# Kernel optimization log

Measured on AMD Instinct MI355X. Metric: run time of the kernel, lower is better.

## Reference

```python
import jax, jax.numpy as jnp
import numpy as np

B, C_IN, H, W = 4, 128, 32, 128   # W must equal out_channels (fc_out acts on last dim)
C_OUT, NUM_HEADS = 128, 2
BN_EPS = 1e-5


def setup_inputs() -> dict:
    key = jax.random.key(0)
    ks = jax.random.split(key, 14)
    s = 0.05  # small init scale for weights
    d = {
        "x": jax.random.normal(ks[0], (B, C_IN, H, W), jnp.float32),
        "wq": jax.random.normal(ks[1], (C_OUT, C_IN), jnp.float32) * s,
        "bq": jax.random.normal(ks[2], (C_OUT,), jnp.float32) * s,
        "wk": jax.random.normal(ks[3], (C_OUT, C_IN), jnp.float32) * s,
        "bk": jax.random.normal(ks[4], (C_OUT,), jnp.float32) * s,
        "wv": jax.random.normal(ks[5], (C_OUT, C_IN), jnp.float32) * s,
        "bv": jax.random.normal(ks[6], (C_OUT,), jnp.float32) * s,
        "fc_w": jax.random.normal(ks[7], (C_OUT, C_OUT), jnp.float32) * s,
        "fc_b": jax.random.normal(ks[8], (C_OUT,), jnp.float32) * s,
        "bn_gamma": jnp.ones((C_OUT,), jnp.float32),
        "bn_beta": jnp.zeros((C_OUT,), jnp.float32),
        "bn_mean": jax.random.normal(ks[9], (C_OUT,), jnp.float32) * 0.1,
        "bn_var": jax.random.uniform(ks[10], (C_OUT,), jnp.float32, 0.5, 1.5),
        "prelu_a": jnp.full((1,), 0.25, jnp.float32),
    }
    return d


def reference(x, wq, bq, wk, bk, wv, bv, fc_w, fc_b,
              bn_gamma, bn_beta, bn_mean, bn_var, prelu_a):
    b, c_in, h, w = x.shape
    c_out = wq.shape[0]
    nh = NUM_HEADS
    dk = c_out // nh
    L = h * w
    xf = x.reshape(b, c_in, L)                                # (B, Cin, L)
    # 1x1 convs == per-token linear projections
    q = jnp.einsum('oi,bil->bol', wq, xf) + bq[:, None]       # (B, Cout, L)
    k = jnp.einsum('oi,bil->bol', wk, xf) + bk[:, None]
    v = jnp.einsum('oi,bil->bol', wv, xf) + bv[:, None]
    Q = q.reshape(b, nh, dk, L)                               # (B, h, d_k, L)
    K = k.reshape(b, nh, dk, L)
    V = v.reshape(b, nh, dk, L)
    # scaled dot-product attention over the L = H*W tokens
    scores = jnp.einsum('bhdl,bhdm->bhlm', Q, K) / jnp.sqrt(jnp.float32(dk))
    attn = jax.nn.softmax(scores, axis=-1)                    # (B, h, L, L)
    out = jnp.einsum('bhlm,bhdm->bhdl', attn, V)              # (B, h, d_k, L)
    out = out.reshape(b, c_out, h, w)                         # (B, Cout, H, W)
    # fc_out: torch Linear on the LAST dim (W == Cout)
    y = jnp.einsum('bchw,ow->bcho', out, fc_w) + fc_b         # (B, Cout, H, W)
    # BatchNorm2d (eval mode: running stats) over channel dim
    inv = jax.lax.rsqrt(bn_var + BN_EPS)
    y = (y - bn_mean[None, :, None, None]) * (inv * bn_gamma)[None, :, None, None] \
        + bn_beta[None, :, None, None]
    # PReLU (single shared slope); dropout is identity in eval
    y = jnp.where(y > 0, y, prelu_a[0] * y)
    return y
```

## Files before the change

### kernel.cpp

```cpp
#include <hip/hip_runtime.h>

typedef _Float16 f16x8 __attribute__((ext_vector_type(8)));
typedef _Float16 f16x4t __attribute__((ext_vector_type(4)));
typedef __fp16 h16x2 __attribute__((ext_vector_type(2)));
typedef float f32x4 __attribute__((ext_vector_type(4)));
typedef float f32x16 __attribute__((ext_vector_type(16)));
typedef unsigned int uint2v __attribute__((ext_vector_type(2)));

#define L_SZ 4096

__device__ __forceinline__ unsigned short f2h(float f) {
    _Float16 h = (_Float16)f;
    return __builtin_bit_cast(unsigned short, h);
}
__device__ __forceinline__ unsigned int pk2(float a, float b) {
    h16x2 p = __builtin_amdgcn_cvt_pkrtz(a, b);
    return __builtin_bit_cast(unsigned int, p);
}
__device__ __forceinline__ float fexp2(float x) {
#if __has_builtin(__builtin_amdgcn_exp2f)
    return __builtin_amdgcn_exp2f(x);
#else
    return exp2f(x);
#endif
}
__device__ __forceinline__ float frcp(float x) {
#if __has_builtin(__builtin_amdgcn_rcpf)
    return __builtin_amdgcn_rcpf(x);
#else
    return 1.0f / x;
#endif
}
__device__ __forceinline__ void async16(unsigned short* lds, const unsigned short* g) {
    __builtin_amdgcn_global_load_lds(
        (const __attribute__((address_space(1))) unsigned int*)g,
        (__attribute__((address_space(3))) unsigned int*)lds, 16, 0, 0);
}

#define SLOT(row, ci) ((((ci) * 64) + ((row) & 32) + (((row) & 31) ^ (ci))) * 8)

__global__ __launch_bounds__(256, 3) void qkv_kernel(
    const float* __restrict__ x,
    const float* __restrict__ wq, const float* __restrict__ wk,
    const float* __restrict__ wv,
    const float* __restrict__ bq, const float* __restrict__ bk,
    const float* __restrict__ bv,
    unsigned short* __restrict__ Qp, unsigned short* __restrict__ Kp,
    unsigned short* __restrict__ Vp)
{
    int raw = blockIdx.x;
    int v = (raw & 7) * 96 + (raw >> 3);
    int tile = v / 3;
    int p = v - tile * 3;
    int bidx = tile >> 6;
    int l0 = (tile & 63) * 64;
    int tid = threadIdx.x;
    int wave = tid >> 6, lane = tid & 63;
    int c = lane & 15, qd = lane >> 4;

    __shared__ __align__(16) unsigned short Ws[128 * 128];
    __shared__ __align__(16) unsigned short Sc[9216];

    const float* wsrc = (p == 0) ? wq : (p == 1 ? wk : wv);
    #pragma unroll
    for (int t = 0; t < 32; ++t) {
        int e2 = tid + t * 256;
        float2 wv2 = *(const float2*)&wsrc[e2 * 2];
        int e = e2 * 2;
        int o = e >> 7, ci = (e & 127) >> 3, j = e & 7;
        *(unsigned int*)&Ws[o * 128 + ((ci ^ (o & 15)) * 8) + j] = pk2(wv2.x, wv2.y);
    }

    unsigned short* Xs = Sc;
    #pragma unroll
    for (int it = 0; it < 8; ++it) {
        int i  = (tid >> 4) + 16 * it;
        int l4 = (tid & 15) * 4;
        const float4 vx = *(const float4*)&x[(bidx * 128 + i) * L_SZ + l0 + l4];
        float vv[4] = {vx.x, vx.y, vx.z, vx.w};
        int ci = i >> 3;
        #pragma unroll
        for (int u = 0; u < 4; ++u) {
            int l = l4 + u;
            Xs[l * 128 + ((ci ^ (l & 15)) * 8) + (i & 7)] = f2h(vv[u]);
        }
    }
    __syncthreads();

    f16x8 afrag[4];
    #pragma unroll
    for (int kc = 0; kc < 4; ++kc) {
        int l = wave * 16 + c;
        int ci = kc * 4 + qd;
        afrag[kc] = *(const f16x8*)&Xs[l * 128 + ((ci ^ (l & 15)) * 8)];
    }
    __syncthreads();

    f32x4 acc[8];
    #pragma unroll
    for (int nt = 0; nt < 8; ++nt) acc[nt] = (f32x4){0.f, 0.f, 0.f, 0.f};

    #pragma unroll
    for (int kc = 0; kc < 4; ++kc) {
        #pragma unroll
        for (int nt = 0; nt < 8; ++nt) {
            int o = nt * 16 + c;
            f16x8 bfrag = *(const f16x8*)&Ws[o * 128 + (((kc * 4 + qd) ^ c) * 8)];
            acc[nt] = __builtin_amdgcn_mfma_f32_16x16x32_f16(afrag[kc], bfrag, acc[nt], 0, 0, 0);
        }
    }

    const float s_q = 0.18033688011f;
    if (p == 0) {
        #pragma unroll
        for (int nt = 0; nt < 8; ++nt) {
            int o = nt * 16 + c;
            int h = o >> 6, d = o & 63;
            #pragma unroll
            for (int r = 0; r < 4; ++r) {
                int l = l0 + wave * 16 + qd * 4 + r;
                Qp[((bidx * 2 + h) * L_SZ + l) * 64 + d] = f2h((acc[nt][r] + bq[o]) * s_q);
            }
        }
    } else if (p == 1) {
        #pragma unroll
        for (int nt = 0; nt < 8; ++nt) {
            int o = nt * 16 + c;
            int h = o >> 6, d = o & 63;
            #pragma unroll
            for (int r = 0; r < 4; ++r) {
                int l = l0 + wave * 16 + qd * 4 + r;
                Kp[((bidx * 2 + h) * L_SZ + l) * 64 + d] = f2h(acc[nt][r] + bk[o]);
            }
        }
    } else {
        unsigned short* Vt = Sc;
        #pragma unroll
        for (int nt = 0; nt < 8; ++nt) {
            int o = nt * 16 + c;
            #pragma unroll
            for (int r = 0; r < 4; ++r) {
                int ll = wave * 16 + qd * 4 + r;
                Vt[o * 72 + ll] = f2h(acc[nt][r] + bv[o]);
            }
        }
        __syncthreads();
        #pragma unroll
        for (int t = 0; t < 2; ++t) {
            int u = tid + t * 256;
            int row = u >> 2;
            int lc = (u & 3) * 16;
            uint4 a0 = *(const uint4*)&Vt[row * 72 + lc];
            uint4 a1 = *(const uint4*)&Vt[row * 72 + lc + 8];
            *(uint4*)&Vp[(size_t)(bidx * 128 + row) * L_SZ + l0 + lc] = a0;
            *(uint4*)&Vp[(size_t)(bidx * 128 + row) * L_SZ + l0 + lc + 8] = a1;
        }
    }
}

__global__ __launch_bounds__(256, 4) void attn_kernel(
    const unsigned short* __restrict__ Qp, const unsigned short* __restrict__ Kp,
    const unsigned short* __restrict__ Vp,
    unsigned short* __restrict__ Opart, float* __restrict__ Mpart, float* __restrict__ Lpart)
{
    int raw = blockIdx.x;
    int blk = (raw & 7) * 128 + (raw >> 3);
    int lt = blk & 31;
    int bh = (blk >> 5) & 7;
    int sp = blk >> 8;
    int l0 = lt * 128;
    int tid = threadIdx.x;
    int wave = tid >> 6, lane = tid & 63;
    int ln = lane & 31, hi = lane >> 5;
    int b = bh >> 1, h = bh & 1;

    __shared__ __align__(16) unsigned short Ks[2][4096];
    __shared__ __align__(16) unsigned short Vs[2][4096];

    const unsigned short* Qb = Qp + (size_t)bh * L_SZ * 64;
    const unsigned short* Kb = Kp + (size_t)bh * L_SZ * 64;
    const unsigned short* Vb = Vp + ((size_t)b * 128 + h * 64) * L_SZ;

    int lq = l0 + wave * 32 + ln;
    f16x8 qf[4];
    #pragma unroll
    for (int kc = 0; kc < 4; ++kc)
        qf[kc] = *(const f16x8*)&Qb[(size_t)lq * 64 + kc * 16 + hi * 8];

    float m_st = -1e30f, lsum = 0.f;
    f32x16 acc0 = {}, acc1 = {};

    int mglob = sp * 1024;
    int ci0 = wave, ci1 = 4 + wave;
    int r0_ = (lane & 32) | ((lane & 31) ^ ci0);
    int r1_ = (lane & 32) | ((lane & 31) ^ ci1);

#define STAGE(t, buf) do {                                                        \
        int m0_ = mglob + (t) * 64;                                               \
        async16(&Ks[buf][(wave * 64) * 8],       &Kb[(size_t)(m0_ + r0_) * 64 + ci0 * 8]); \
        async16(&Ks[buf][(256 + wave * 64) * 8], &Kb[(size_t)(m0_ + r1_) * 64 + ci1 * 8]); \
        async16(&Vs[buf][(wave * 64) * 8],       &Vb[(size_t)r0_ * L_SZ + m0_ + ci0 * 8]); \
        async16(&Vs[buf][(256 + wave * 64) * 8], &Vb[(size_t)r1_ * L_SZ + m0_ + ci1 * 8]); \
    } while (0)

    STAGE(0, 0);

    for (int it = 0; it < 16; ++it) {
        int cur = it & 1;
        __syncthreads();
        if (it < 15) STAGE(it + 1, cur ^ 1);

        __builtin_amdgcn_s_setprio(1);
        f32x16 s0 = {}, s1 = {};
        #pragma unroll
        for (int kc = 0; kc < 4; ++kc) {
            int cd = kc * 2 + hi;
            f16x8 k0 = *(const f16x8*)&Ks[cur][SLOT(ln, cd)];
            f16x8 k1 = *(const f16x8*)&Ks[cur][SLOT(32 + ln, cd)];
            s0 = __builtin_amdgcn_mfma_f32_32x32x16_f16(k0, qf[kc], s0, 0, 0, 0);
            s1 = __builtin_amdgcn_mfma_f32_32x32x16_f16(k1, qf[kc], s1, 0, 0, 0);
        }

        float t[8];
        #pragma unroll
        for (int r = 0; r < 8; ++r)
            t[r] = fmaxf(fmaxf(s0[r], s0[r + 8]), s1[r]);
        #pragma unroll
        for (int r = 0; r < 4; ++r)
            t[r] = fmaxf(fmaxf(t[r], t[r + 4]), s1[8 + r]);
        float m01 = fmaxf(fmaxf(t[0], t[1]), s1[12]);
        float m23 = fmaxf(fmaxf(t[2], t[3]), s1[13]);
        float mx = fmaxf(fmaxf(m01, m23), fmaxf(s1[14], s1[15]));
        mx = fmaxf(mx, __shfl_xor(mx, 32));

        if (!__all(mx <= m_st + 8.0f)) {
            float mnew = fmaxf(m_st, mx);
            float alpha = fexp2(m_st - mnew);
            m_st = mnew;
            lsum *= alpha;
            #pragma unroll
            for (int r = 0; r < 16; ++r) { acc0[r] *= alpha; acc1[r] *= alpha; }
        }
        float rs0 = 0.f, rs1 = 0.f, rs2 = 0.f, rs3 = 0.f;
        #pragma unroll
        for (int r = 0; r < 4; ++r) {
            float p0 = fexp2(s0[r]      - m_st); s0[r]      = p0; rs0 += p0;
            float p1 = fexp2(s0[r + 4]  - m_st); s0[r + 4]  = p1; rs1 += p1;
            float p2 = fexp2(s0[r + 8]  - m_st); s0[r + 8]  = p2; rs2 += p2;
            float p3 = fexp2(s0[r + 12] - m_st); s0[r + 12] = p3; rs3 += p3;
        }
        #pragma unroll
        for (int r = 0; r < 4; ++r) {
            float p0 = fexp2(s1[r]      - m_st); s1[r]      = p0; rs0 += p0;
            float p1 = fexp2(s1[r + 4]  - m_st); s1[r + 4]  = p1; rs1 += p1;
            float p2 = fexp2(s1[r + 8]  - m_st); s1[r + 8]  = p2; rs2 += p2;
            float p3 = fexp2(s1[r + 12] - m_st); s1[r + 12] = p3; rs3 += p3;
        }
        lsum += (rs0 + rs1) + (rs2 + rs3);

        #pragma unroll
        for (int kc = 0; kc < 4; ++kc) {
            unsigned int a0, a1, a2, a3;
            if (kc == 0) {
                a0 = pk2(s0[0], s0[1]);  a1 = pk2(s0[2], s0[3]);
                a2 = pk2(s0[4], s0[5]);  a3 = pk2(s0[6], s0[7]);
            } else if (kc == 1) {
                a0 = pk2(s0[8], s0[9]);  a1 = pk2(s0[10], s0[11]);
                a2 = pk2(s0[12], s0[13]); a3 = pk2(s0[14], s0[15]);
            } else if (kc == 2) {
                a0 = pk2(s1[0], s1[1]);  a1 = pk2(s1[2], s1[3]);
                a2 = pk2(s1[4], s1[5]);  a3 = pk2(s1[6], s1[7]);
            } else {
                a0 = pk2(s1[8], s1[9]);  a1 = pk2(s1[10], s1[11]);
                a2 = pk2(s1[12], s1[13]); a3 = pk2(s1[14], s1[15]);
            }
            uint2v r02 = __builtin_amdgcn_permlane32_swap(a0, a2, false, false);
            uint2v r13 = __builtin_amdgcn_permlane32_swap(a1, a3, false, false);
            uint4 pw; pw.x = r02[0]; pw.y = r13[0]; pw.z = r02[1]; pw.w = r13[1];
            f16x8 pf = __builtin_bit_cast(f16x8, pw);
            int cd = kc * 2 + hi;
            f16x8 v0 = *(const f16x8*)&Vs[cur][SLOT(ln, cd)];
            f16x8 v1 = *(const f16x8*)&Vs[cur][SLOT(32 + ln, cd)];
            acc0 = __builtin_amdgcn_mfma_f32_32x32x16_f16(v0, pf, acc0, 0, 0, 0);
            acc1 = __builtin_amdgcn_mfma_f32_32x32x16_f16(v1, pf, acc1, 0, 0, 0);
        }
        __builtin_amdgcn_s_setprio(0);
    }
#undef STAGE

    float l_tot = lsum + __shfl_xor(lsum, 32);
    unsigned short* Ow = Opart + (size_t)(sp * 8 + bh) * 64 * 4096;
    #pragma unroll
    for (int r = 0; r < 16; ++r) {
        int d0 = (r & 3) + 8 * (r >> 2) + 4 * hi;
        Ow[(size_t)d0 * 4096 + lq] = f2h(acc0[r]);
        Ow[(size_t)(32 + d0) * 4096 + lq] = f2h(acc1[r]);
    }
    if (hi == 0) {
        Mpart[(sp * 8 + bh) * 4096 + lq] = m_st;
        Lpart[(sp * 8 + bh) * 4096 + lq] = l_tot;
    }
}

__global__ __launch_bounds__(256, 2) void fc_kernel(
    const unsigned short* __restrict__ Opart, const float* __restrict__ Mp,
    const float* __restrict__ Lp, const float* __restrict__ fcw_f,
    const float* __restrict__ fc_b, const float* __restrict__ bn_g,
    const float* __restrict__ bn_b, const float* __restrict__ bn_m,
    const float* __restrict__ bn_v, const float* __restrict__ prelu_a,
    float* __restrict__ out)
{
    int raw = blockIdx.x;
    int blk = (raw & 7) * 64 + (raw >> 3);
    int r0 = blk * 32;
    int tid = threadIdx.x;
    int c0 = blk & 127;
    int bh = blk >> 6;
    int d = c0 & 63;

    int wave = tid >> 6, lane = tid & 63;
    int c = lane & 15, qd = lane >> 4;
    int rw = r0 + (wave >> 1) * 16;
    int o0 = (wave & 1) * 64;
    int hh = (rw + c) & 31;

    __shared__ __align__(16) unsigned short Fw[128 * 128];
    __shared__ __align__(16) unsigned short SclU[4096 * 4];

    uint4 ovr[4][4];
    #pragma unroll
    for (int kc = 0; kc < 4; ++kc) {
        int w0 = kc * 32 + qd * 8;
        #pragma unroll
        for (int s = 0; s < 4; ++s)
            ovr[kc][s] = *(const uint4*)&Opart[(size_t)(s * 8 + bh) * 262144 + (size_t)d * 4096 + hh * 128 + w0];
    }

    #pragma unroll
    for (int t = 0; t < 16; ++t) {
        int l = tid + t * 256;
        float m0 = Mp[(0 * 8 + bh) * 4096 + l], m1 = Mp[(1 * 8 + bh) * 4096 + l];
        float m2 = Mp[(2 * 8 + bh) * 4096 + l], m3 = Mp[(3 * 8 + bh) * 4096 + l];
        float mx = fmaxf(fmaxf(m0, m1), fmaxf(m2, m3));
        float a0 = fexp2(m0 - mx), a1 = fexp2(m1 - mx);
        float a2 = fexp2(m2 - mx), a3 = fexp2(m3 - mx);
        float den = a0 * Lp[(0 * 8 + bh) * 4096 + l] + a1 * Lp[(1 * 8 + bh) * 4096 + l]
                  + a2 * Lp[(2 * 8 + bh) * 4096 + l] + a3 * Lp[(3 * 8 + bh) * 4096 + l];
        float inv = frcp(den);
        int hl = l >> 7, ww = l & 127;
        int slot = hl * 128 + ((ww + hl) & 127);
        uint2 sc;
        sc.x = pk2(a0 * inv, a1 * inv);
        sc.y = pk2(a2 * inv, a3 * inv);
        *(uint2*)&SclU[slot * 4] = sc;
    }
    #pragma unroll
    for (int t = 0; t < 32; ++t) {
        int e2 = tid + t * 256;
        float2 v = *(const float2*)&fcw_f[e2 * 2];
        int e = e2 * 2;
        int o = e >> 7, ci = (e & 127) >> 3, j = e & 7;
        *(unsigned int*)&Fw[o * 128 + ((ci ^ (o & 15)) * 8) + j] = pk2(v.x, v.y);
    }
    __syncthreads();

    f16x8 af[4];
    #pragma unroll
    for (int kc = 0; kc < 4; ++kc) {
        int w0 = kc * 32 + qd * 8;
        f16x8 ov0 = __builtin_bit_cast(f16x8, ovr[kc][0]);
        f16x8 ov1 = __builtin_bit_cast(f16x8, ovr[kc][1]);
        f16x8 ov2 = __builtin_bit_cast(f16x8, ovr[kc][2]);
        f16x8 ov3 = __builtin_bit_cast(f16x8, ovr[kc][3]);
        #pragma unroll
        for (int j = 0; j < 8; ++j) {
            int slot = hh * 128 + ((w0 + j + hh) & 127);
            f16x4t sc = *(const f16x4t*)&SclU[slot * 4];
            float v = (float)ov0[j] * (float)sc[0] + (float)ov1[j] * (float)sc[1]
                    + (float)ov2[j] * (float)sc[2] + (float)ov3[j] * (float)sc[3];
            af[kc][j] = (_Float16)v;
        }
    }

    f32x4 acc[4];
    #pragma unroll
    for (int nt = 0; nt < 4; ++nt) acc[nt] = (f32x4){0.f, 0.f, 0.f, 0.f};
    #pragma unroll
    for (int kc = 0; kc < 4; ++kc) {
        #pragma unroll
        for (int nt = 0; nt < 4; ++nt) {
            int o = o0 + nt * 16 + c;
            f16x8 bf = *(const f16x8*)&Fw[o * 128 + (((kc * 4 + qd) ^ c) * 8)];
            acc[nt] = __builtin_amdgcn_mfma_f32_16x16x32_f16(af[kc], bf, acc[nt], 0, 0, 0);
        }
    }

    float pa = prelu_a[0];
    float g  = bn_g[c0] * rsqrtf(bn_v[c0] + 1e-5f);
    float mn = bn_m[c0], bt = bn_b[c0];
    #pragma unroll
    for (int r = 0; r < 4; ++r) {
        int orow = rw + qd * 4 + r;
        #pragma unroll
        for (int nt = 0; nt < 4; ++nt) {
            int o = o0 + nt * 16 + c;
            float y = (acc[nt][r] + fc_b[o] - mn) * g + bt;
            y = y > 0.f ? y : pa * y;
            out[(size_t)orow * 128 + o] = y;
        }
    }
}

extern "C" void kernel_launch(void* const* d_in, const int* in_sizes, int n_in,
                              void* d_out, int out_size, void* d_ws, size_t ws_size,
                              hipStream_t stream) {
    const float* x     = (const float*)d_in[0];
    const float* wq    = (const float*)d_in[1];
    const float* bq    = (const float*)d_in[2];
    const float* wk    = (const float*)d_in[3];
    const float* bk    = (const float*)d_in[4];
    const float* wv    = (const float*)d_in[5];
    const float* bv    = (const float*)d_in[6];
    const float* fcw_f = (const float*)d_in[7];
    const float* fcb   = (const float*)d_in[8];
    const float* bn_g  = (const float*)d_in[9];
    const float* bn_b  = (const float*)d_in[10];
    const float* bn_m  = (const float*)d_in[11];
    const float* bn_v  = (const float*)d_in[12];
    const float* pa    = (const float*)d_in[13];
    float* out = (float*)d_out;

    unsigned short* Qp  = (unsigned short*)d_ws;
    unsigned short* Kp  = Qp + 8 * L_SZ * 64;
    unsigned short* Vp  = Kp + 8 * L_SZ * 64;
    unsigned short* Opart = Vp + 8 * L_SZ * 64;
    float* Mpart = (float*)(Opart + 4 * 8 * 64 * L_SZ);
    float* Lpart = Mpart + 4 * 8 * L_SZ;

    hipLaunchKernelGGL(qkv_kernel,  dim3(768),  dim3(256), 0, stream,
                       x, wq, wk, wv, bq, bk, bv, Qp, Kp, Vp);
    hipLaunchKernelGGL(attn_kernel, dim3(1024), dim3(256), 0, stream,
                       Qp, Kp, Vp, Opart, Mpart, Lpart);
    hipLaunchKernelGGL(fc_kernel,   dim3(512),  dim3(256), 0, stream,
                       Opart, Mpart, Lpart, fcw_f, fcb, bn_g, bn_b, bn_m, bn_v, pa, out);
}
```

Measured before the change: 158.5 us.

## Precompute fp16 weight and softmax-scale images in prep kernels, async-load into LDS

Adds a prep kernel that converts the QKV and fc weights to swizzled fp16 images once, and a scl_kernel that computes the per-split softmax merge scales once per (batch, head). qkv_kernel and fc_kernel now copy these images into LDS with global_load_lds async copies instead of redundantly converting fp32 data in every block. Q/K outputs are staged through LDS so they can be written with coalesced 16-byte stores. This adds two extra kernel launches and some workspace traffic.

```diff
diff --git a/kernel.cpp b/kernel.cpp
--- a/kernel.cpp
+++ b/kernel.cpp
@@ -39,10 +39,29 @@
 
 #define SLOT(row, ci) ((((ci) * 64) + ((row) & 32) + (((row) & 31) ^ (ci))) * 8)
 
+__global__ __launch_bounds__(256) void prep_kernel(
+    const float* __restrict__ wq, const float* __restrict__ wk,
+    const float* __restrict__ wv, const float* __restrict__ fcw,
+    unsigned short* __restrict__ Wimg, unsigned short* __restrict__ Fimg)
+{
+    int e2 = blockIdx.x * 256 + threadIdx.x;
+    if (e2 < 24576) {
+        const float* src = (e2 < 8192) ? wq : (e2 < 16384 ? wk : wv);
+        float2 v = *(const float2*)&src[(e2 * 2) & 16383];
+        int e = e2 * 2;
+        int o = e >> 7, ci = (e & 127) >> 3, j = e & 7;
+        *(unsigned int*)&Wimg[o * 128 + ((ci ^ (o & 15)) * 8) + j] = pk2(v.x, v.y);
+    } else {
+        int fe = (e2 - 24576) * 2;
+        float2 v = *(const float2*)&fcw[fe];
+        int o = fe >> 7, ci = (fe & 127) >> 3, j = fe & 7;
+        *(unsigned int*)&Fimg[o * 128 + ((ci ^ (o & 15)) * 8) + j] = pk2(v.x, v.y);
+    }
+}
+
 __global__ __launch_bounds__(256, 3) void qkv_kernel(
     const float* __restrict__ x,
-    const float* __restrict__ wq, const float* __restrict__ wk,
-    const float* __restrict__ wv,
+    const unsigned short* __restrict__ Wimg,
     const float* __restrict__ bq, const float* __restrict__ bk,
     const float* __restrict__ bv,
     unsigned short* __restrict__ Qp, unsigned short* __restrict__ Kp,
@@ -61,15 +80,10 @@
     __shared__ __align__(16) unsigned short Ws[128 * 128];
     __shared__ __align__(16) unsigned short Sc[9216];
 
-    const float* wsrc = (p == 0) ? wq : (p == 1 ? wk : wv);
-    #pragma unroll
-    for (int t = 0; t < 32; ++t) {
-        int e2 = tid + t * 256;
-        float2 wv2 = *(const float2*)&wsrc[e2 * 2];
-        int e = e2 * 2;
-        int o = e >> 7, ci = (e & 127) >> 3, j = e & 7;
-        *(unsigned int*)&Ws[o * 128 + ((ci ^ (o & 15)) * 8) + j] = pk2(wv2.x, wv2.y);
-    }
+    const unsigned short* wsrc = Wimg + p * 16384;
+    #pragma unroll
+    for (int t = 0; t < 8; ++t)
+        async16(&Ws[(t * 256 + wave * 64) * 8], &wsrc[(size_t)(t * 256 + wave * 64 + lane) * 8]);
 
     unsigned short* Xs = Sc;
     #pragma unroll
@@ -111,27 +125,30 @@
     }
 
     const float s_q = 0.18033688011f;
-    if (p == 0) {
+    if (p < 2) {
+        const float* bias = (p == 0) ? bq : bk;
+        unsigned short* Ot = Sc;
         #pragma unroll
         for (int nt = 0; nt < 8; ++nt) {
             int o = nt * 16 + c;
-            int h = o >> 6, d = o & 63;
+            float bo = bias[o];
             #pragma unroll
             for (int r = 0; r < 4; ++r) {
-                int l = l0 + wave * 16 + qd * 4 + r;
-                Qp[((bidx * 2 + h) * L_SZ + l) * 64 + d] = f2h((acc[nt][r] + bq[o]) * s_q);
+                int ll = wave * 16 + qd * 4 + r;
+                float val = acc[nt][r] + bo;
+                if (p == 0) val *= s_q;
+                Ot[ll * 144 + o] = f2h(val);
             }
         }
-    } else if (p == 1) {
-        #pragma unroll
-        for (int nt = 0; nt < 8; ++nt) {
-            int o = nt * 16 + c;
-            int h = o >> 6, d = o & 63;
-            #pragma unroll
-            for (int r = 0; r < 4; ++r) {
-                int l = l0 + wave * 16 + qd * 4 + r;
-                Kp[((bidx * 2 + h) * L_SZ + l) * 64 + d] = f2h(acc[nt][r] + bk[o]);
-            }
+        __syncthreads();
+        unsigned short* dst = (p == 0) ? Qp : Kp;
+        #pragma unroll
+        for (int t = 0; t < 4; ++t) {
+            int u = tid + t * 256;
+            int row = u >> 4, col = (u & 15) * 8;
+            int h = col >> 6, d = col & 63;
+            uint4 a = *(const uint4*)&Ot[row * 144 + col];
+            *(uint4*)&dst[((size_t)(bidx * 2 + h) * L_SZ + l0 + row) * 64 + d] = a;
         }
     } else {
         unsigned short* Vt = Sc;
@@ -302,9 +319,32 @@
     }
 }
 
+__global__ __launch_bounds__(256) void scl_kernel(
+    const float* __restrict__ Mp, const float* __restrict__ Lp,
+    unsigned short* __restrict__ SclImg)
+{
+    int gid = blockIdx.x * 256 + threadIdx.x;
+    int bh = gid >> 12, l = gid & 4095;
+    float m0 = Mp[(0 * 8 + bh) * 4096 + l], m1 = Mp[(1 * 8 + bh) * 4096 + l];
+    float m2 = Mp[(2 * 8 + bh) * 4096 + l], m3 = Mp[(3 * 8 + bh) * 4096 + l];
+    float mx = fmaxf(fmaxf(m0, m1), fmaxf(m2, m3));
+    float a0 = fexp2(m0 - mx), a1 = fexp2(m1 - mx);
+    float a2 = fexp2(m2 - mx), a3 = fexp2(m3 - mx);
+    float den = a0 * Lp[(0 * 8 + bh) * 4096 + l] + a1 * Lp[(1 * 8 + bh) * 4096 + l]
+              + a2 * Lp[(2 * 8 + bh) * 4096 + l] + a3 * Lp[(3 * 8 + bh) * 4096 + l];
+    float inv = frcp(den);
+    int hl = l >> 7, ww = l & 127;
+    int slot = hl * 128 + ((ww + hl) & 127);
+    uint2 sc;
+    sc.x = pk2(a0 * inv, a1 * inv);
+    sc.y = pk2(a2 * inv, a3 * inv);
+    *(uint2*)&SclImg[((size_t)bh * 4096 + slot) * 4] = sc;
+}
+
 __global__ __launch_bounds__(256, 2) void fc_kernel(
-    const unsigned short* __restrict__ Opart, const float* __restrict__ Mp,
-    const float* __restrict__ Lp, const float* __restrict__ fcw_f,
+    const unsigned short* __restrict__ Opart,
+    const unsigned short* __restrict__ SclImg,
+    const unsigned short* __restrict__ Fimg,
     const float* __restrict__ fc_b, const float* __restrict__ bn_g,
     const float* __restrict__ bn_b, const float* __restrict__ bn_m,
     const float* __restrict__ bn_v, const float* __restrict__ prelu_a,
@@ -327,6 +367,15 @@
     __shared__ __align__(16) unsigned short Fw[128 * 128];
     __shared__ __align__(16) unsigned short SclU[4096 * 4];
 
+    #pragma unroll
+    for (int t = 0; t < 8; ++t)
+        async16(&SclU[(t * 256 + wave * 64) * 8],
+                &SclImg[(size_t)bh * 16384 + (size_t)(t * 256 + wave * 64 + lane) * 8]);
+    #pragma unroll
+    for (int t = 0; t < 8; ++t)
+        async16(&Fw[(t * 256 + wave * 64) * 8],
+                &Fimg[(size_t)(t * 256 + wave * 64 + lane) * 8]);
+
     uint4 ovr[4][4];
     #pragma unroll
     for (int kc = 0; kc < 4; ++kc) {
@@ -334,33 +383,6 @@
         #pragma unroll
         for (int s = 0; s < 4; ++s)
             ovr[kc][s] = *(const uint4*)&Opart[(size_t)(s * 8 + bh) * 262144 + (size_t)d * 4096 + hh * 128 + w0];
-    }
-
-    #pragma unroll
-    for (int t = 0; t < 16; ++t) {
-        int l = tid + t * 256;
-        float m0 = Mp[(0 * 8 + bh) * 4096 + l], m1 = Mp[(1 * 8 + bh) * 4096 + l];
-        float m2 = Mp[(2 * 8 + bh) * 4096 + l], m3 = Mp[(3 * 8 + bh) * 4096 + l];
-        float mx = fmaxf(fmaxf(m0, m1), fmaxf(m2, m3));
-        float a0 = fexp2(m0 - mx), a1 = fexp2(m1 - mx);
-        float a2 = fexp2(m2 - mx), a3 = fexp2(m3 - mx);
-        float den = a0 * Lp[(0 * 8 + bh) * 4096 + l] + a1 * Lp[(1 * 8 + bh) * 4096 + l]
-                  + a2 * Lp[(2 * 8 + bh) * 4096 + l] + a3 * Lp[(3 * 8 + bh) * 4096 + l];
-        float inv = frcp(den);
-        int hl = l >> 7, ww = l & 127;
-        int slot = hl * 128 + ((ww + hl) & 127);
-        uint2 sc;
-        sc.x = pk2(a0 * inv, a1 * inv);
-        sc.y = pk2(a2 * inv, a3 * inv);
-        *(uint2*)&SclU[slot * 4] = sc;
-    }
-    #pragma unroll
-    for (int t = 0; t < 32; ++t) {
-        int e2 = tid + t * 256;
-        float2 v = *(const float2*)&fcw_f[e2 * 2];
-        int e = e2 * 2;
-        int o = e >> 7, ci = (e & 127) >> 3, j = e & 7;
-        *(unsigned int*)&Fw[o * 128 + ((ci ^ (o & 15)) * 8) + j] = pk2(v.x, v.y);
     }
     __syncthreads();
 
@@ -436,11 +458,18 @@
     unsigned short* Opart = Vp + 8 * L_SZ * 64;
     float* Mpart = (float*)(Opart + 4 * 8 * 64 * L_SZ);
     float* Lpart = Mpart + 4 * 8 * L_SZ;
-
+    unsigned short* Wimg   = (unsigned short*)(Lpart + 4 * 8 * L_SZ);
+    unsigned short* Fimg   = Wimg + 384 * 128;
+    unsigned short* SclImg = Fimg + 128 * 128;
+
+    hipLaunchKernelGGL(prep_kernel, dim3(128),  dim3(256), 0, stream,
+                       wq, wk, wv, fcw_f, Wimg, Fimg);
     hipLaunchKernelGGL(qkv_kernel,  dim3(768),  dim3(256), 0, stream,
-                       x, wq, wk, wv, bq, bk, bv, Qp, Kp, Vp);
+                       x, Wimg, bq, bk, bv, Qp, Kp, Vp);
     hipLaunchKernelGGL(attn_kernel, dim3(1024), dim3(256), 0, stream,
                        Qp, Kp, Vp, Opart, Mpart, Lpart);
+    hipLaunchKernelGGL(scl_kernel,  dim3(128),  dim3(256), 0, stream,
+                       Mpart, Lpart, SclImg);
     hipLaunchKernelGGL(fc_kernel,   dim3(512),  dim3(256), 0, stream,
-                       Opart, Mpart, Lpart, fcw_f, fcb, bn_g, bn_b, bn_m, bn_v, pa, out);
-}
+                       Opart, SclImg, Fimg, fcb, bn_g, bn_b, bn_m, bn_v, pa, out);
+}
```

New measurement: 158.6 us. No clear change (+0.1%).
